# Optimization experiments

Measured on AMD Instinct MI355X. Metric: run time of the kernel, lower is better.

Reference implementation:

```python
import jax, jax.numpy as jnp
import numpy as np

EPS_NORM = 1e-12   # torch F.normalize eps
EPS_BN = 1e-5      # BatchNorm1d eps
NEG_SLOPE = 0.01   # LeakyReLU default


def _l2_normalize(x, axis):
    # torch F.normalize: x / max(||x||, eps)
    n = jnp.sqrt(jnp.sum(x * x, axis=axis, keepdims=True))
    return x / jnp.maximum(n, EPS_NORM)


def setup_inputs() -> dict:
    key = jax.random.key(0)
    k1, k2, k3, k4, k5, k6, k7 = jax.random.split(key, 7)
    B, C, N, M, OUT = 8, 128, 4096, 4096, 128
    return {
        "input": jax.random.normal(k1, (B, C, N), dtype=jnp.float32),
        "target_g": jax.random.normal(k2, (B, C, M), dtype=jnp.float32),
        "weight": jax.random.normal(k3, (C, OUT), dtype=jnp.float32) * (1.0 / np.sqrt(OUT)),
        "gamma": jax.random.normal(k4, (OUT,), dtype=jnp.float32),
        "beta": jax.random.normal(k5, (OUT,), dtype=jnp.float32),
        "running_mean": jax.random.normal(k6, (OUT,), dtype=jnp.float32),
        "running_var": jax.random.uniform(k7, (OUT,), dtype=jnp.float32, minval=0.5, maxval=1.5),
    }


def reference(input, target_g, weight, gamma, beta, running_mean, running_var):
    # input: [B, C, N], target_g: [B, C, M]
    # cosine-similarity adjacency: [B, M, N]
    tg = _l2_normalize(target_g, axis=1)
    inp_n = _l2_normalize(input, axis=1)
    adj = jnp.einsum('bcm,bcn->bmn', tg, inp_n)
    adj = jax.nn.softmax(adj, axis=-1)
    # aggregate: [B, M, C]
    agg = jnp.einsum('bmn,bcn->bmc', adj, input)
    # project: [B, M, OUT] -> permute to [B, OUT, M]
    out = jnp.einsum('bmc,co->bom', agg, weight)
    # LeakyReLU then BatchNorm1d (eval mode, running stats)
    out = jnp.where(out >= 0, out, NEG_SLOPE * out)
    inv = jax.lax.rsqrt(running_var + EPS_BN)
    out = (out - running_mean[None, :, None]) * (inv * gamma)[None, :, None] + beta[None, :, None]
    return out
```

## Files before the change

### kernel.cpp

```cpp
#include <hip/hip_runtime.h>
#include <hip/hip_bf16.h>

#define BATCH 8
#define CDIM 128
#define NDIM 4096

typedef __bf16 bf16x8 __attribute__((ext_vector_type(8)));
typedef float f32x4 __attribute__((ext_vector_type(4)));
typedef float f32x16 __attribute__((ext_vector_type(16)));
typedef unsigned u32x4 __attribute__((ext_vector_type(4)));

#define QT_OFF 0u
#define KT_OFF 8388608u
#define VB_OFF 16777216u
#define WT_OFF 25165824u
#define SC_OFF (WT_OFF + 32768u)
#define BI_OFF (SC_OFF + 512u)

__device__ __forceinline__ f32x4 mfma16(bf16x8 a, bf16x8 b, f32x4 c) {
    return __builtin_amdgcn_mfma_f32_16x16x32_bf16(a, b, c, 0, 0, 0);
}
__device__ __forceinline__ f32x16 mfma32(bf16x8 a, bf16x8 b, f32x16 c) {
    return __builtin_amdgcn_mfma_f32_32x32x16_bf16(a, b, c, 0, 0, 0);
}

__device__ __forceinline__ unsigned pack2bf(float a, float b) {
    unsigned short ul = __builtin_bit_cast(unsigned short, (__bf16)a);
    unsigned short uh = __builtin_bit_cast(unsigned short, (__bf16)b);
    return (unsigned)ul | ((unsigned)uh << 16);
}

__device__ __forceinline__ void glds16(const void* g, void* l) {
    __builtin_amdgcn_global_load_lds((__attribute__((address_space(1))) void*)(void*)g,
                                     (__attribute__((address_space(3))) void*)l, 16, 0, 0);
}

__device__ __forceinline__ void pls32(unsigned& a, unsigned& b) {
    asm("v_permlane32_swap_b32 %0, %1" : "+v"(a), "+v"(b));
}

__global__ __launch_bounds__(256) void prep_nt(const float* __restrict__ input,
                                               const float* __restrict__ tg,
                                               const float* __restrict__ wgt,
                                               const float* __restrict__ gamma,
                                               const float* __restrict__ beta,
                                               const float* __restrict__ mean,
                                               const float* __restrict__ var,
                                               void* __restrict__ ws) {
    __shared__ float Tt[64][129];
    __shared__ float psum[4][64];
    __shared__ float rn[64];
    const int n0 = blockIdx.x * 64;
    const int b  = blockIdx.y;
    const int tid = threadIdx.x;
    const float* src = (blockIdx.z == 0 ? input : tg) + (size_t)b * CDIM * NDIM;

    #pragma unroll
    for (int i = 0; i < 8; ++i) {
        int f = tid + i * 256;
        int c = f >> 4, j4 = f & 15;
        float4 v = *(const float4*)(src + (size_t)c * NDIM + n0 + j4 * 4);
        Tt[j4 * 4 + 0][c] = v.x;
        Tt[j4 * 4 + 1][c] = v.y;
        Tt[j4 * 4 + 2][c] = v.z;
        Tt[j4 * 4 + 3][c] = v.w;
    }
    __syncthreads();
    {
        int j = tid & 63, part = tid >> 6;
        float ss = 0.f;
        #pragma unroll 8
        for (int c = part * 32; c < part * 32 + 32; ++c) { float x = Tt[j][c]; ss += x * x; }
        psum[part][j] = ss;
    }
    __syncthreads();
    if (tid < 64) {
        float s = psum[0][tid] + psum[1][tid] + psum[2][tid] + psum[3][tid];
        rn[tid] = 1.0f / fmaxf(sqrtf(s), 1e-12f);
    }
    __syncthreads();

    __hip_bfloat16* dstT = (__hip_bfloat16*)((char*)ws + (blockIdx.z == 0 ? KT_OFF : QT_OFF))
                           + ((size_t)b * NDIM + n0) * CDIM;
    #pragma unroll
    for (int i = 0; i < 8; ++i) {
        int f = tid + i * 256;
        int j = f >> 5, c4 = f & 31;
        float r = rn[j];
        float4 v = *(const float4*)&Tt[j][c4 * 4];
        uint2 pk; pk.x = pack2bf(v.x * r, v.y * r); pk.y = pack2bf(v.z * r, v.w * r);
        *(uint2*)((unsigned short*)dstT + (size_t)j * CDIM + c4 * 4) = pk;
    }
    if (blockIdx.z == 0) {
        __hip_bfloat16* vb = (__hip_bfloat16*)((char*)ws + VB_OFF) + (size_t)b * CDIM * NDIM + n0;
        #pragma unroll
        for (int i = 0; i < 8; ++i) {
            int f = tid + i * 256;
            int c = f >> 4, j4 = f & 15;
            float x0 = Tt[j4 * 4 + 0][c], x1 = Tt[j4 * 4 + 1][c];
            float x2 = Tt[j4 * 4 + 2][c], x3 = Tt[j4 * 4 + 3][c];
            uint2 pv; pv.x = pack2bf(x0, x1); pv.y = pack2bf(x2, x3);
            *(uint2*)((unsigned short*)vb + (size_t)c * NDIM + j4 * 4) = pv;
        }
    } else if (blockIdx.x == 0 && b == 0) {
        __hip_bfloat16* wT = (__hip_bfloat16*)((char*)ws + WT_OFF);
        float* sc = (float*)((char*)ws + SC_OFF);
        float* bi = (float*)((char*)ws + BI_OFF);
        #pragma unroll
        for (int i = 0; i < 64; ++i) {
            int f = tid + i * 256;
            int c = f >> 7, o = f & 127;
            wT[o * 128 + c] = __hip_bfloat16(wgt[c * 128 + o]);
        }
        if (tid < 128) {
            float inv = rsqrtf(var[tid] + 1e-5f);
            float s = inv * gamma[tid];
            sc[tid] = s;
            bi[tid] = beta[tid] - mean[tid] * s;
        }
    }
}

__global__ __launch_bounds__(512, 2) void flash6(const void* __restrict__ ws_,
                                                 float* __restrict__ out) {
    extern __shared__ char smem[];
    const char* ws = (const char*)ws_;
    const __hip_bfloat16* Qt = (const __hip_bfloat16*)(ws + QT_OFF);
    const __hip_bfloat16* Kt = (const __hip_bfloat16*)(ws + KT_OFF);
    const __hip_bfloat16* Vb = (const __hip_bfloat16*)(ws + VB_OFF);
    const __hip_bfloat16* wT = (const __hip_bfloat16*)(ws + WT_OFF);
    const float* scale = (const float*)(ws + SC_OFF);
    const float* bias  = (const float*)(ws + BI_OFF);

    const int bx = blockIdx.x;
    const int b  = bx & 7;
    const int m0 = (bx >> 3) * 128;
    const int tid = threadIdx.x;
    const int w = tid >> 6, lane = tid & 63;
    const int hf = lane >> 5;
    const int l31 = lane & 31;
    const int nt = w & 1;
    const int mt = w >> 1;

    const char* kgb = (const char*)(Kt + (size_t)b * NDIM * CDIM);
    const char* vgb = (const char*)(Vb + (size_t)b * CDIM * NDIM);

    bf16x8 qb[8];
    {
        const char* qrow = (const char*)Qt + ((size_t)b * NDIM + m0 + mt * 32 + l31) * 256 + hf * 16;
        #pragma unroll
        for (int s = 0; s < 8; ++s) qb[s] = *(const bf16x8*)(qrow + s * 32);
    }

    unsigned kOff[8];
    {
        int nn = nt * 64 + l31;
        #pragma unroll
        for (int s = 0; s < 8; ++s)
            kOff[s] = nn * 256 + (((2 * s + hf) ^ (nn & 15)) * 16);
    }
    unsigned vOff[2][4];
    #pragma unroll
    for (int t = 0; t < 2; ++t)
        #pragma unroll
        for (int ca = 0; ca < 4; ++ca) {
            int c = ca * 32 + l31;
            vOff[t][ca] = 32768 + c * 256 + (((nt * 8 + t * 2 + hf) ^ (c & 15)) * 16);
        }

    const char* kSrc[4]; const char* vSrc[4];
    unsigned kDst[4], vDst[4];
    #pragma unroll
    for (int i = 0; i < 4; ++i) {
        int slot = i * 512 + tid;
        int r = slot >> 4, j = slot & 15;
        kSrc[i] = kgb + r * 256 + ((j ^ (r & 15)) * 16);
        kDst[i] = i * 8192 + w * 1024;
        vSrc[i] = vgb + (size_t)r * 8192 + ((j ^ (r & 15)) * 16);
        vDst[i] = 32768 + i * 8192 + w * 1024;
    }

    f32x16 oacc[4];
    #pragma unroll
    for (int ca = 0; ca < 4; ++ca)
        #pragma unroll
        for (int i = 0; i < 16; ++i) oacc[ca][i] = 0.f;
    float lacc = 0.f;

    #pragma unroll
    for (int i = 0; i < 4; ++i) { glds16(kSrc[i], smem + kDst[i]); kSrc[i] += 32768; }
    #pragma unroll
    for (int i = 0; i < 4; ++i) { glds16(vSrc[i], smem + vDst[i]); vSrc[i] += 256; }

    auto softmax_pf = [&](const f32x16& s, bf16x8* pf) {
        unsigned d[8];
        float lsum = 0.f;
        #pragma unroll
        for (int rq = 0; rq < 4; ++rq) {
            float e0 = __expf(s[rq * 4 + 0] - 1.0f);
            float e1 = __expf(s[rq * 4 + 1] - 1.0f);
            float e2 = __expf(s[rq * 4 + 2] - 1.0f);
            float e3 = __expf(s[rq * 4 + 3] - 1.0f);
            lsum += (e0 + e1) + (e2 + e3);
            d[rq * 2 + 0] = pack2bf(e0, e1);
            d[rq * 2 + 1] = pack2bf(e2, e3);
        }
        lacc += lsum;
        #pragma unroll
        for (int t = 0; t < 2; ++t) {
            pls32(d[4 * t + 0], d[4 * t + 2]);
            pls32(d[4 * t + 1], d[4 * t + 3]);
            u32x4 tv;
            tv.x = d[4 * t + 0]; tv.y = d[4 * t + 1];
            tv.z = d[4 * t + 2]; tv.w = d[4 * t + 3];
            pf[t] = __builtin_bit_cast(bf16x8, tv);
        }
    };

    auto body = [&](const unsigned bo, const bool do_pref) {
        asm volatile("s_waitcnt vmcnt(0) lgkmcnt(0)\ns_barrier" ::: "memory");
        if (do_pref) {
            const unsigned obo = bo ^ 65536u;
            #pragma unroll
            for (int i = 0; i < 4; ++i) { glds16(kSrc[i], smem + (obo + kDst[i])); kSrc[i] += 32768; }
            #pragma unroll
            for (int i = 0; i < 4; ++i) { glds16(vSrc[i], smem + (obo + vDst[i])); vSrc[i] += 256; }
        }
        const char* base = smem + bo;

        f32x16 st0;
        #pragma unroll
        for (int i = 0; i < 16; ++i) st0[i] = 0.f;
        #pragma unroll
        for (int s = 0; s < 8; ++s) {
            bf16x8 kf = *(const bf16x8*)(base + kOff[s]);
            st0 = mfma32(kf, qb[s], st0);
        }
        bf16x8 pf0[2];
        softmax_pf(st0, pf0);

        f32x16 st1;
        #pragma unroll
        for (int i = 0; i < 16; ++i) st1[i] = 0.f;
        #pragma unroll
        for (int s = 0; s < 8; ++s) {
            bf16x8 kf = *(const bf16x8*)(base + kOff[s] + 8192);
            st1 = mfma32(kf, qb[s], st1);
        }

        #pragma unroll
        for (int t = 0; t < 2; ++t)
            #pragma unroll
            for (int ca = 0; ca < 4; ++ca) {
                bf16x8 vf = *(const bf16x8*)(base + vOff[t][ca]);
                oacc[ca] = mfma32(vf, pf0[t], oacc[ca]);
            }

        bf16x8 pf1[2];
        softmax_pf(st1, pf1);

        #pragma unroll
        for (int t = 0; t < 2; ++t)
            #pragma unroll
            for (int ca = 0; ca < 4; ++ca) {
                bf16x8 vf = *(const bf16x8*)(base + (vOff[t][ca] ^ 64u));
                oacc[ca] = mfma32(vf, pf1[t], oacc[ca]);
            }
    };

    for (int ii = 0; ii < 16; ++ii) {
        body(0u, true);
        body(65536u, ii != 15);
    }

    float lw = lacc + __shfl_xor(lacc, 32, 64);
    __syncthreads();
    float* lLds = (float*)(smem + 65536);
    if (lane < 32) lLds[w * 32 + lane] = lw;
    if (w & 1) {
        float4* dst = (float4*)smem + (w >> 1) * 1024 + lane;
        #pragma unroll
        for (int ca = 0; ca < 4; ++ca)
            #pragma unroll
            for (int rq = 0; rq < 4; ++rq) {
                float4 t = { oacc[ca][rq * 4 + 0], oacc[ca][rq * 4 + 1],
                             oacc[ca][rq * 4 + 2], oacc[ca][rq * 4 + 3] };
                dst[(ca * 4 + rq) * 64] = t;
            }
    }
    __syncthreads();
    char* sAgg = smem + 67584;
    if (!(w & 1)) {
        float linv = 1.0f / (lLds[w * 32 + l31] + lLds[(w + 1) * 32 + l31]);
        const float4* srcp = (const float4*)smem + (w >> 1) * 1024 + lane;
        int m = (w >> 1) * 32 + l31;
        char* aggRow = sAgg + m * 256;
        const int mx = (m & 7) << 1;
        #pragma unroll
        for (int ca = 0; ca < 4; ++ca)
            #pragma unroll
            for (int rq = 0; rq < 4; ++rq) {
                float4 ov = srcp[(ca * 4 + rq) * 64];
                float v0 = (oacc[ca][rq * 4 + 0] + ov.x) * linv;
                float v1 = (oacc[ca][rq * 4 + 1] + ov.y) * linv;
                float v2 = (oacc[ca][rq * 4 + 2] + ov.z) * linv;
                float v3 = (oacc[ca][rq * 4 + 3] + ov.w) * linv;
                int cq = ca * 8 + rq * 2 + hf;
                uint2 pk; pk.x = pack2bf(v0, v1); pk.y = pack2bf(v2, v3);
                *(uint2*)(aggRow + ((cq ^ mx) * 8)) = pk;
            }
    }
    __syncthreads();

    const int li = lane & 15, q = lane >> 4;
    const int pm = w * 16 + li;
    f32x4 racc[8];
    #pragma unroll
    for (int ob = 0; ob < 8; ++ob) { racc[ob][0]=0.f; racc[ob][1]=0.f; racc[ob][2]=0.f; racc[ob][3]=0.f; }
    #pragma unroll
    for (int ks = 0; ks < 4; ++ks) {
        int slot8 = ((ks * 4 + q) * 2) ^ ((li & 7) << 1);
        bf16x8 af = *(const bf16x8*)(sAgg + pm * 256 + slot8 * 8);
        #pragma unroll
        for (int ob = 0; ob < 8; ++ob) {
            bf16x8 wf = *(const bf16x8*)((const char*)wT + (ob * 16 + li) * 256 + ks * 64 + q * 16);
            racc[ob] = mfma16(af, wf, racc[ob]);
        }
    }

    float* sRes = (float*)smem;
    #pragma unroll
    for (int ob = 0; ob < 8; ++ob) {
        int oo = ob * 16 + li;
        float sc = scale[oo], bi = bias[oo];
        #pragma unroll
        for (int r = 0; r < 4; ++r) {
            float v = racc[ob][r];
            v = (v >= 0.0f) ? v : 0.01f * v;
            v = v * sc + bi;
            sRes[oo * 132 + w * 16 + q * 4 + r] = v;
        }
    }
    __syncthreads();

    float* outb = out + (size_t)b * CDIM * NDIM + m0;
    #pragma unroll
    for (int i = 0; i < 8; ++i) {
        int f = tid + i * 512;
        int o = f >> 5, mq = f & 31;
        *(float4*)(outb + (size_t)o * NDIM + mq * 4) = *(const float4*)(sRes + o * 132 + mq * 4);
    }
}

extern "C" void kernel_launch(void* const* d_in, const int* in_sizes, int n_in,
                              void* d_out, int out_size, void* d_ws, size_t ws_size,
                              hipStream_t stream) {
    const float* input  = (const float*)d_in[0];
    const float* tg     = (const float*)d_in[1];
    const float* weight = (const float*)d_in[2];
    const float* gamma  = (const float*)d_in[3];
    const float* beta   = (const float*)d_in[4];
    const float* rmean  = (const float*)d_in[5];
    const float* rvar   = (const float*)d_in[6];
    float* out = (float*)d_out;

    (void)in_sizes; (void)n_in; (void)out_size; (void)ws_size;

    hipFuncSetAttribute(reinterpret_cast<const void*>(flash6),
                        hipFuncAttributeMaxDynamicSharedMemorySize, 131072);

    dim3 gprep(NDIM / 64, BATCH, 2);
    prep_nt<<<gprep, 256, 0, stream>>>(input, tg, weight, gamma, beta, rmean, rvar, d_ws);
    flash6<<<dim3(256), 512, 131072, stream>>>(d_ws, out);
}
```

Measured before the change: 181.0 us.

## Double flash kernel block to 1024 threads with 4-way key split per row tile

Doubles the attention kernel's block size to 16 waves, so each 32-row query tile is split across four key sub-ranges instead of two. Each wave now computes one score tile per step instead of two. K/V tiles are stored in LDS in a new unswizzled layout, with each thread issuing half as many global-to-LDS copies. The extra split adds a two-stage cross-wave reduction through LDS and more barriers. The unswizzled LDS layout may cause bank conflicts, and 1024 threads at 128KB LDS can limit occupancy.

```diff
diff --git a/kernel.cpp b/kernel.cpp
--- a/kernel.cpp
+++ b/kernel.cpp
@@ -121,8 +121,8 @@
     }
 }
 
-__global__ __launch_bounds__(512, 2) void flash6(const void* __restrict__ ws_,
-                                                 float* __restrict__ out) {
+__global__ __launch_bounds__(1024, 4) void flash8(const void* __restrict__ ws_,
+                                                  float* __restrict__ out) {
     extern __shared__ char smem[];
     const char* ws = (const char*)ws_;
     const __hip_bfloat16* Qt = (const __hip_bfloat16*)(ws + QT_OFF);
@@ -139,8 +139,8 @@
     const int w = tid >> 6, lane = tid & 63;
     const int hf = lane >> 5;
     const int l31 = lane & 31;
-    const int nt = w & 1;
-    const int mt = w >> 1;
+    const int nt = w & 3;
+    const int mt = w >> 2;
 
     const char* kgb = (const char*)(Kt + (size_t)b * NDIM * CDIM);
     const char* vgb = (const char*)(Vb + (size_t)b * CDIM * NDIM);
@@ -152,33 +152,18 @@
         for (int s = 0; s < 8; ++s) qb[s] = *(const bf16x8*)(qrow + s * 32);
     }
 
-    unsigned kOff[8];
-    {
-        int nn = nt * 64 + l31;
-        #pragma unroll
-        for (int s = 0; s < 8; ++s)
-            kOff[s] = nn * 256 + (((2 * s + hf) ^ (nn & 15)) * 16);
-    }
-    unsigned vOff[2][4];
-    #pragma unroll
-    for (int t = 0; t < 2; ++t)
-        #pragma unroll
-        for (int ca = 0; ca < 4; ++ca) {
-            int c = ca * 32 + l31;
-            vOff[t][ca] = 32768 + c * 256 + (((nt * 8 + t * 2 + hf) ^ (c & 15)) * 16);
-        }
-
-    const char* kSrc[4]; const char* vSrc[4];
-    unsigned kDst[4], vDst[4];
-    #pragma unroll
-    for (int i = 0; i < 4; ++i) {
-        int slot = i * 512 + tid;
-        int r = slot >> 4, j = slot & 15;
-        kSrc[i] = kgb + r * 256 + ((j ^ (r & 15)) * 16);
-        kDst[i] = i * 8192 + w * 1024;
-        vSrc[i] = vgb + (size_t)r * 8192 + ((j ^ (r & 15)) * 16);
-        vDst[i] = 32768 + i * 8192 + w * 1024;
-    }
+    const unsigned kAddr = (nt * 32 + l31) * 16 + hf * 2048;
+    const unsigned vAddr = 65536 + nt * 8192 + hf * 2048 + l31 * 16;
+
+    unsigned kSrcLane[2], vSrcLane[2];
+    #pragma unroll
+    for (int i = 0; i < 2; ++i) {
+        int slot = i * 1024 + tid;
+        int rr = slot & 127, ch = slot >> 7;
+        kSrcLane[i] = rr * 256 + ch * 16;
+        vSrcLane[i] = rr * 8192 + ch * 16;
+    }
+    const unsigned dstU = w * 1024;
 
     f32x16 oacc[4];
     #pragma unroll
@@ -188,9 +173,11 @@
     float lacc = 0.f;
 
     #pragma unroll
-    for (int i = 0; i < 4; ++i) { glds16(kSrc[i], smem + kDst[i]); kSrc[i] += 32768; }
-    #pragma unroll
-    for (int i = 0; i < 4; ++i) { glds16(vSrc[i], smem + vDst[i]); vSrc[i] += 256; }
+    for (int i = 0; i < 2; ++i) glds16(kgb + kSrcLane[i], smem + (i * 16384 + dstU));
+    #pragma unroll
+    for (int i = 0; i < 2; ++i) glds16(vgb + vSrcLane[i], smem + (65536 + i * 16384 + dstU));
+    unsigned kOffG = 32768;
+    unsigned vOffG = 256;
 
     auto softmax_pf = [&](const f32x16& s, bf16x8* pf) {
         unsigned d[8];
@@ -220,65 +207,45 @@
     auto body = [&](const unsigned bo, const bool do_pref) {
         asm volatile("s_waitcnt vmcnt(0) lgkmcnt(0)\ns_barrier" ::: "memory");
         if (do_pref) {
-            const unsigned obo = bo ^ 65536u;
-            #pragma unroll
-            for (int i = 0; i < 4; ++i) { glds16(kSrc[i], smem + (obo + kDst[i])); kSrc[i] += 32768; }
-            #pragma unroll
-            for (int i = 0; i < 4; ++i) { glds16(vSrc[i], smem + (obo + vDst[i])); vSrc[i] += 256; }
-        }
-        const char* base = smem + bo;
-
-        f32x16 st0;
-        #pragma unroll
-        for (int i = 0; i < 16; ++i) st0[i] = 0.f;
+            const unsigned obo = bo ^ 32768u;
+            #pragma unroll
+            for (int i = 0; i < 2; ++i) glds16(kgb + kOffG + kSrcLane[i], smem + (obo + i * 16384 + dstU));
+            #pragma unroll
+            for (int i = 0; i < 2; ++i) glds16(vgb + vOffG + vSrcLane[i], smem + (65536 + obo + i * 16384 + dstU));
+            kOffG += 32768;
+            vOffG += 256;
+        }
+
+        f32x16 st;
+        #pragma unroll
+        for (int i = 0; i < 16; ++i) st[i] = 0.f;
         #pragma unroll
         for (int s = 0; s < 8; ++s) {
-            bf16x8 kf = *(const bf16x8*)(base + kOff[s]);
-            st0 = mfma32(kf, qb[s], st0);
-        }
-        bf16x8 pf0[2];
-        softmax_pf(st0, pf0);
-
-        f32x16 st1;
-        #pragma unroll
-        for (int i = 0; i < 16; ++i) st1[i] = 0.f;
-        #pragma unroll
-        for (int s = 0; s < 8; ++s) {
-            bf16x8 kf = *(const bf16x8*)(base + kOff[s] + 8192);
-            st1 = mfma32(kf, qb[s], st1);
-        }
+            bf16x8 kf = *(const bf16x8*)(smem + bo + kAddr + s * 4096);
+            st = mfma32(kf, qb[s], st);
+        }
+
+        bf16x8 pf[2];
+        softmax_pf(st, pf);
 
         #pragma unroll
         for (int t = 0; t < 2; ++t)
             #pragma unroll
             for (int ca = 0; ca < 4; ++ca) {
-                bf16x8 vf = *(const bf16x8*)(base + vOff[t][ca]);
-                oacc[ca] = mfma32(vf, pf0[t], oacc[ca]);
-            }
-
-        bf16x8 pf1[2];
-        softmax_pf(st1, pf1);
-
-        #pragma unroll
-        for (int t = 0; t < 2; ++t)
-            #pragma unroll
-            for (int ca = 0; ca < 4; ++ca) {
-                bf16x8 vf = *(const bf16x8*)(base + (vOff[t][ca] ^ 64u));
-                oacc[ca] = mfma32(vf, pf1[t], oacc[ca]);
+                bf16x8 vf = *(const bf16x8*)(smem + bo + vAddr + t * 4096 + ca * 512);
+                oacc[ca] = mfma32(vf, pf[t], oacc[ca]);
             }
     };
 
     for (int ii = 0; ii < 16; ++ii) {
         body(0u, true);
-        body(65536u, ii != 15);
+        body(32768u, ii != 15);
     }
 
     float lw = lacc + __shfl_xor(lacc, 32, 64);
     __syncthreads();
-    float* lLds = (float*)(smem + 65536);
-    if (lane < 32) lLds[w * 32 + lane] = lw;
-    if (w & 1) {
-        float4* dst = (float4*)smem + (w >> 1) * 1024 + lane;
+    if (nt >= 2) {
+        float4* dst = (float4*)smem + (mt * 2 + (nt - 2)) * 1024 + lane;
         #pragma unroll
         for (int ca = 0; ca < 4; ++ca)
             #pragma unroll
@@ -289,11 +256,40 @@
             }
     }
     __syncthreads();
+    if (nt < 2) {
+        const float4* srcp = (const float4*)smem + (mt * 2 + nt) * 1024 + lane;
+        #pragma unroll
+        for (int ca = 0; ca < 4; ++ca)
+            #pragma unroll
+            for (int rq = 0; rq < 4; ++rq) {
+                float4 ov = srcp[(ca * 4 + rq) * 64];
+                oacc[ca][rq * 4 + 0] += ov.x;
+                oacc[ca][rq * 4 + 1] += ov.y;
+                oacc[ca][rq * 4 + 2] += ov.z;
+                oacc[ca][rq * 4 + 3] += ov.w;
+            }
+    }
+    __syncthreads();
+    float* lLds = (float*)(smem + 65536);
+    if (lane < 32) lLds[w * 32 + lane] = lw;
+    if (nt == 1) {
+        float4* dst = (float4*)smem + mt * 1024 + lane;
+        #pragma unroll
+        for (int ca = 0; ca < 4; ++ca)
+            #pragma unroll
+            for (int rq = 0; rq < 4; ++rq) {
+                float4 t = { oacc[ca][rq * 4 + 0], oacc[ca][rq * 4 + 1],
+                             oacc[ca][rq * 4 + 2], oacc[ca][rq * 4 + 3] };
+                dst[(ca * 4 + rq) * 64] = t;
+            }
+    }
+    __syncthreads();
     char* sAgg = smem + 67584;
-    if (!(w & 1)) {
-        float linv = 1.0f / (lLds[w * 32 + l31] + lLds[(w + 1) * 32 + l31]);
-        const float4* srcp = (const float4*)smem + (w >> 1) * 1024 + lane;
-        int m = (w >> 1) * 32 + l31;
+    if (nt == 0) {
+        float linv = 1.0f / (lLds[(mt * 4 + 0) * 32 + l31] + lLds[(mt * 4 + 1) * 32 + l31]
+                           + lLds[(mt * 4 + 2) * 32 + l31] + lLds[(mt * 4 + 3) * 32 + l31]);
+        const float4* srcp = (const float4*)smem + mt * 1024 + lane;
+        int m = mt * 32 + l31;
         char* aggRow = sAgg + m * 256;
         const int mx = (m & 7) << 1;
         #pragma unroll
@@ -313,40 +309,42 @@
     __syncthreads();
 
     const int li = lane & 15, q = lane >> 4;
-    const int pm = w * 16 + li;
-    f32x4 racc[8];
-    #pragma unroll
-    for (int ob = 0; ob < 8; ++ob) { racc[ob][0]=0.f; racc[ob][1]=0.f; racc[ob][2]=0.f; racc[ob][3]=0.f; }
-    #pragma unroll
-    for (int ks = 0; ks < 4; ++ks) {
-        int slot8 = ((ks * 4 + q) * 2) ^ ((li & 7) << 1);
-        bf16x8 af = *(const bf16x8*)(sAgg + pm * 256 + slot8 * 8);
+    if (w < 8) {
+        const int pm = w * 16 + li;
+        f32x4 racc[8];
+        #pragma unroll
+        for (int ob = 0; ob < 8; ++ob) { racc[ob][0]=0.f; racc[ob][1]=0.f; racc[ob][2]=0.f; racc[ob][3]=0.f; }
+        #pragma unroll
+        for (int ks = 0; ks < 4; ++ks) {
+            int slot8 = ((ks * 4 + q) * 2) ^ ((li & 7) << 1);
+            bf16x8 af = *(const bf16x8*)(sAgg + pm * 256 + slot8 * 8);
+            #pragma unroll
+            for (int ob = 0; ob < 8; ++ob) {
+                bf16x8 wf = *(const bf16x8*)((const char*)wT + (ob * 16 + li) * 256 + ks * 64 + q * 16);
+                racc[ob] = mfma16(af, wf, racc[ob]);
+            }
+        }
+        float* sRes = (float*)smem;
         #pragma unroll
         for (int ob = 0; ob < 8; ++ob) {
-            bf16x8 wf = *(const bf16x8*)((const char*)wT + (ob * 16 + li) * 256 + ks * 64 + q * 16);
-            racc[ob] = mfma16(af, wf, racc[ob]);
-        }
-    }
-
-    float* sRes = (float*)smem;
-    #pragma unroll
-    for (int ob = 0; ob < 8; ++ob) {
-        int oo = ob * 16 + li;
-        float sc = scale[oo], bi = bias[oo];
-        #pragma unroll
-        for (int r = 0; r < 4; ++r) {
-            float v = racc[ob][r];
-            v = (v >= 0.0f) ? v : 0.01f * v;
-            v = v * sc + bi;
-            sRes[oo * 132 + w * 16 + q * 4 + r] = v;
-        }
-    }
-    __syncthreads();
-
+            int oo = ob * 16 + li;
+            float sc = scale[oo], bi = bias[oo];
+            #pragma unroll
+            for (int r = 0; r < 4; ++r) {
+                float v = racc[ob][r];
+                v = (v >= 0.0f) ? v : 0.01f * v;
+                v = v * sc + bi;
+                sRes[oo * 132 + w * 16 + q * 4 + r] = v;
+            }
+        }
+    }
+    __syncthreads();
+
+    const float* sRes = (const float*)smem;
     float* outb = out + (size_t)b * CDIM * NDIM + m0;
     #pragma unroll
-    for (int i = 0; i < 8; ++i) {
-        int f = tid + i * 512;
+    for (int i = 0; i < 4; ++i) {
+        int f = tid + i * 1024;
         int o = f >> 5, mq = f & 31;
         *(float4*)(outb + (size_t)o * NDIM + mq * 4) = *(const float4*)(sRes + o * 132 + mq * 4);
     }
@@ -366,10 +364,10 @@
 
     (void)in_sizes; (void)n_in; (void)out_size; (void)ws_size;
 
-    hipFuncSetAttribute(reinterpret_cast<const void*>(flash6),
+    hipFuncSetAttribute(reinterpret_cast<const void*>(flash8),
                         hipFuncAttributeMaxDynamicSharedMemorySize, 131072);
 
     dim3 gprep(NDIM / 64, BATCH, 2);
     prep_nt<<<gprep, 256, 0, stream>>>(input, tg, weight, gamma, beta, rmean, rvar, d_ws);
-    flash6<<<dim3(256), 512, 131072, stream>>>(d_ws, out);
-}
+    flash8<<<dim3(256), 1024, 131072, stream>>>(d_ws, out);
+}
```

New measurement: 241.9 us. 33.6% more time.

## Split prep into norm and pack kernels, add MFMA setprio hints

Applied to the files above, without the earlier changes.

The single prep kernel is split in two. A column-norm kernel reads the inputs with coalesced strided loads and writes reciprocal norms into the output buffer, used as scratch. A pack kernel then transposes and writes the bf16 V copy inside its first load loop, which removes the LDS reduction phase and two barriers. The flash kernel raises wave priority around its MFMA loops with s_setprio, so matrix work is favoured over softmax on other waves. The cost is an extra kernel launch and a second full read of the fp32 inputs.

```diff
diff --git a/kernel.cpp b/kernel.cpp
--- a/kernel.cpp
+++ b/kernel.cpp
@@ -39,22 +39,64 @@
     asm("v_permlane32_swap_b32 %0, %1" : "+v"(a), "+v"(b));
 }
 
-__global__ __launch_bounds__(256) void prep_nt(const float* __restrict__ input,
-                                               const float* __restrict__ tg,
-                                               const float* __restrict__ wgt,
-                                               const float* __restrict__ gamma,
-                                               const float* __restrict__ beta,
-                                               const float* __restrict__ mean,
-                                               const float* __restrict__ var,
-                                               void* __restrict__ ws) {
+__global__ __launch_bounds__(256) void prep_norm(const float* __restrict__ input,
+                                                 const float* __restrict__ tg,
+                                                 const float* __restrict__ wgt,
+                                                 const float* __restrict__ gamma,
+                                                 const float* __restrict__ beta,
+                                                 const float* __restrict__ mean,
+                                                 const float* __restrict__ var,
+                                                 float* __restrict__ rn,
+                                                 void* __restrict__ ws) {
+    __shared__ float ps[128];
+    const int b = blockIdx.y, z = blockIdx.z;
+    const int tid = threadIdx.x;
+    const int nl = tid & 127, ch = tid >> 7;
+    const int n = blockIdx.x * 128 + nl;
+    const float* srcp = (z ? tg : input) + ((size_t)b * CDIM + ch * 64) * NDIM + n;
+    float ss = 0.f;
+    #pragma unroll 16
+    for (int c = 0; c < 64; ++c) { float x = srcp[(size_t)c * NDIM]; ss = fmaf(x, x, ss); }
+    if (ch) ps[nl] = ss;
+    __syncthreads();
+    if (!ch) {
+        float t = ss + ps[nl];
+        rn[((size_t)z * BATCH + b) * NDIM + n] = 1.0f / fmaxf(sqrtf(t), 1e-12f);
+    }
+    if (z == 1 && blockIdx.x == 0 && b == 0) {
+        __hip_bfloat16* wT = (__hip_bfloat16*)((char*)ws + WT_OFF);
+        float* sc = (float*)((char*)ws + SC_OFF);
+        float* bi = (float*)((char*)ws + BI_OFF);
+        #pragma unroll 4
+        for (int i = 0; i < 64; ++i) {
+            int f = tid + i * 256;
+            int o = f >> 7, c = f & 127;
+            wT[o * 128 + c] = __hip_bfloat16(wgt[c * 128 + o]);
+        }
+        if (tid < 128) {
+            float inv = rsqrtf(var[tid] + 1e-5f);
+            float s = inv * gamma[tid];
+            sc[tid] = s;
+            bi[tid] = beta[tid] - mean[tid] * s;
+        }
+    }
+}
+
+__global__ __launch_bounds__(256) void prep_pack(const float* __restrict__ input,
+                                                 const float* __restrict__ tg,
+                                                 const float* __restrict__ rn,
+                                                 void* __restrict__ ws) {
     __shared__ float Tt[64][129];
-    __shared__ float psum[4][64];
-    __shared__ float rn[64];
+    __shared__ float rf[64];
     const int n0 = blockIdx.x * 64;
     const int b  = blockIdx.y;
+    const int z  = blockIdx.z;
     const int tid = threadIdx.x;
-    const float* src = (blockIdx.z == 0 ? input : tg) + (size_t)b * CDIM * NDIM;
-
+    const float* src = (z == 0 ? input : tg) + (size_t)b * CDIM * NDIM;
+
+    if (tid < 64) rf[tid] = rn[((size_t)z * BATCH + b) * NDIM + n0 + tid];
+
+    __hip_bfloat16* vb = (__hip_bfloat16*)((char*)ws + VB_OFF) + (size_t)b * CDIM * NDIM + n0;
     #pragma unroll
     for (int i = 0; i < 8; ++i) {
         int f = tid + i * 256;
@@ -64,60 +106,23 @@
         Tt[j4 * 4 + 1][c] = v.y;
         Tt[j4 * 4 + 2][c] = v.z;
         Tt[j4 * 4 + 3][c] = v.w;
-    }
-    __syncthreads();
-    {
-        int j = tid & 63, part = tid >> 6;
-        float ss = 0.f;
-        #pragma unroll 8
-        for (int c = part * 32; c < part * 32 + 32; ++c) { float x = Tt[j][c]; ss += x * x; }
-        psum[part][j] = ss;
-    }
-    __syncthreads();
-    if (tid < 64) {
-        float s = psum[0][tid] + psum[1][tid] + psum[2][tid] + psum[3][tid];
-        rn[tid] = 1.0f / fmaxf(sqrtf(s), 1e-12f);
-    }
-    __syncthreads();
-
-    __hip_bfloat16* dstT = (__hip_bfloat16*)((char*)ws + (blockIdx.z == 0 ? KT_OFF : QT_OFF))
+        if (z == 0) {
+            uint2 pv; pv.x = pack2bf(v.x, v.y); pv.y = pack2bf(v.z, v.w);
+            *(uint2*)((unsigned short*)vb + (size_t)c * NDIM + j4 * 4) = pv;
+        }
+    }
+    __syncthreads();
+
+    __hip_bfloat16* dstT = (__hip_bfloat16*)((char*)ws + (z == 0 ? KT_OFF : QT_OFF))
                            + ((size_t)b * NDIM + n0) * CDIM;
     #pragma unroll
     for (int i = 0; i < 8; ++i) {
         int f = tid + i * 256;
         int j = f >> 5, c4 = f & 31;
-        float r = rn[j];
+        float r = rf[j];
         float4 v = *(const float4*)&Tt[j][c4 * 4];
         uint2 pk; pk.x = pack2bf(v.x * r, v.y * r); pk.y = pack2bf(v.z * r, v.w * r);
         *(uint2*)((unsigned short*)dstT + (size_t)j * CDIM + c4 * 4) = pk;
-    }
-    if (blockIdx.z == 0) {
-        __hip_bfloat16* vb = (__hip_bfloat16*)((char*)ws + VB_OFF) + (size_t)b * CDIM * NDIM + n0;
-        #pragma unroll
-        for (int i = 0; i < 8; ++i) {
-            int f = tid + i * 256;
-            int c = f >> 4, j4 = f & 15;
-            float x0 = Tt[j4 * 4 + 0][c], x1 = Tt[j4 * 4 + 1][c];
-            float x2 = Tt[j4 * 4 + 2][c], x3 = Tt[j4 * 4 + 3][c];
-            uint2 pv; pv.x = pack2bf(x0, x1); pv.y = pack2bf(x2, x3);
-            *(uint2*)((unsigned short*)vb + (size_t)c * NDIM + j4 * 4) = pv;
-        }
-    } else if (blockIdx.x == 0 && b == 0) {
-        __hip_bfloat16* wT = (__hip_bfloat16*)((char*)ws + WT_OFF);
-        float* sc = (float*)((char*)ws + SC_OFF);
-        float* bi = (float*)((char*)ws + BI_OFF);
-        #pragma unroll
-        for (int i = 0; i < 64; ++i) {
-            int f = tid + i * 256;
-            int c = f >> 7, o = f & 127;
-            wT[o * 128 + c] = __hip_bfloat16(wgt[c * 128 + o]);
-        }
-        if (tid < 128) {
-            float inv = rsqrtf(var[tid] + 1e-5f);
-            float s = inv * gamma[tid];
-            sc[tid] = s;
-            bi[tid] = beta[tid] - mean[tid] * s;
-        }
     }
 }
 
@@ -231,17 +236,20 @@
         f32x16 st0;
         #pragma unroll
         for (int i = 0; i < 16; ++i) st0[i] = 0.f;
+        __builtin_amdgcn_s_setprio(1);
         #pragma unroll
         for (int s = 0; s < 8; ++s) {
             bf16x8 kf = *(const bf16x8*)(base + kOff[s]);
             st0 = mfma32(kf, qb[s], st0);
         }
+        __builtin_amdgcn_s_setprio(0);
         bf16x8 pf0[2];
         softmax_pf(st0, pf0);
 
         f32x16 st1;
         #pragma unroll
         for (int i = 0; i < 16; ++i) st1[i] = 0.f;
+        __builtin_amdgcn_s_setprio(1);
         #pragma unroll
         for (int s = 0; s < 8; ++s) {
             bf16x8 kf = *(const bf16x8*)(base + kOff[s] + 8192);
@@ -255,10 +263,12 @@
                 bf16x8 vf = *(const bf16x8*)(base + vOff[t][ca]);
                 oacc[ca] = mfma32(vf, pf0[t], oacc[ca]);
             }
+        __builtin_amdgcn_s_setprio(0);
 
         bf16x8 pf1[2];
         softmax_pf(st1, pf1);
 
+        __builtin_amdgcn_s_setprio(1);
         #pragma unroll
         for (int t = 0; t < 2; ++t)
             #pragma unroll
@@ -266,6 +276,7 @@
                 bf16x8 vf = *(const bf16x8*)(base + (vOff[t][ca] ^ 64u));
                 oacc[ca] = mfma32(vf, pf1[t], oacc[ca]);
             }
+        __builtin_amdgcn_s_setprio(0);
     };
 
     for (int ii = 0; ii < 16; ++ii) {
@@ -369,7 +380,10 @@
     hipFuncSetAttribute(reinterpret_cast<const void*>(flash6),
                         hipFuncAttributeMaxDynamicSharedMemorySize, 131072);
 
-    dim3 gprep(NDIM / 64, BATCH, 2);
-    prep_nt<<<gprep, 256, 0, stream>>>(input, tg, weight, gamma, beta, rmean, rvar, d_ws);
+    float* rnbuf = out;
+
+    prep_norm<<<dim3(NDIM / 128, BATCH, 2), 256, 0, stream>>>(
+        input, tg, weight, gamma, beta, rmean, rvar, rnbuf, d_ws);
+    prep_pack<<<dim3(NDIM / 64, BATCH, 2), 256, 0, stream>>>(input, tg, rnbuf, d_ws);
     flash6<<<dim3(256), 512, 131072, stream>>>(d_ws, out);
 }
```

New measurement: 187.1 us. 3.4% more time.

## Fuse prep and flash kernels into one cooperative launch with grid sync

Applied to the files above, without the earlier changes.

Merges the normalization/transpose prep kernel into the main attention kernel. Each of the 256 blocks now processes four 64-column prep tiles, then all blocks meet at a cooperative grid-wide barrier before the flash stage. This removes a kernel launch and the gap between the two kernels. In exchange, the prep work runs on only 256 blocks instead of 1024 and needs a grid barrier, which may lower memory parallelism in the prep phase.

```diff
diff --git a/kernel.cpp b/kernel.cpp
--- a/kernel.cpp
+++ b/kernel.cpp
@@ -1,5 +1,8 @@
 #include <hip/hip_runtime.h>
 #include <hip/hip_bf16.h>
+#include <hip/hip_cooperative_groups.h>
+
+namespace cg = cooperative_groups;
 
 #define BATCH 8
 #define CDIM 128
@@ -39,92 +42,110 @@
     asm("v_permlane32_swap_b32 %0, %1" : "+v"(a), "+v"(b));
 }
 
-__global__ __launch_bounds__(256) void prep_nt(const float* __restrict__ input,
-                                               const float* __restrict__ tg,
-                                               const float* __restrict__ wgt,
-                                               const float* __restrict__ gamma,
-                                               const float* __restrict__ beta,
-                                               const float* __restrict__ mean,
-                                               const float* __restrict__ var,
-                                               void* __restrict__ ws) {
-    __shared__ float Tt[64][129];
-    __shared__ float psum[4][64];
-    __shared__ float rn[64];
-    const int n0 = blockIdx.x * 64;
-    const int b  = blockIdx.y;
+__global__ __launch_bounds__(512, 2) void fused(const float* __restrict__ input,
+                                                const float* __restrict__ tg,
+                                                const float* __restrict__ wgt,
+                                                const float* __restrict__ gamma,
+                                                const float* __restrict__ beta,
+                                                const float* __restrict__ mean,
+                                                const float* __restrict__ var,
+                                                void* __restrict__ wsv,
+                                                float* __restrict__ out) {
+    extern __shared__ char smem[];
+    char* ws = (char*)wsv;
+    const int bx = blockIdx.x;
+    const int b  = bx & 7;
     const int tid = threadIdx.x;
-    const float* src = (blockIdx.z == 0 ? input : tg) + (size_t)b * CDIM * NDIM;
-
-    #pragma unroll
-    for (int i = 0; i < 8; ++i) {
-        int f = tid + i * 256;
-        int c = f >> 4, j4 = f & 15;
-        float4 v = *(const float4*)(src + (size_t)c * NDIM + n0 + j4 * 4);
-        Tt[j4 * 4 + 0][c] = v.x;
-        Tt[j4 * 4 + 1][c] = v.y;
-        Tt[j4 * 4 + 2][c] = v.z;
-        Tt[j4 * 4 + 3][c] = v.w;
-    }
-    __syncthreads();
+
     {
-        int j = tid & 63, part = tid >> 6;
-        float ss = 0.f;
-        #pragma unroll 8
-        for (int c = part * 32; c < part * 32 + 32; ++c) { float x = Tt[j][c]; ss += x * x; }
-        psum[part][j] = ss;
-    }
-    __syncthreads();
-    if (tid < 64) {
-        float s = psum[0][tid] + psum[1][tid] + psum[2][tid] + psum[3][tid];
-        rn[tid] = 1.0f / fmaxf(sqrtf(s), 1e-12f);
-    }
-    __syncthreads();
-
-    __hip_bfloat16* dstT = (__hip_bfloat16*)((char*)ws + (blockIdx.z == 0 ? KT_OFF : QT_OFF))
-                           + ((size_t)b * NDIM + n0) * CDIM;
-    #pragma unroll
-    for (int i = 0; i < 8; ++i) {
-        int f = tid + i * 256;
-        int j = f >> 5, c4 = f & 31;
-        float r = rn[j];
-        float4 v = *(const float4*)&Tt[j][c4 * 4];
-        uint2 pk; pk.x = pack2bf(v.x * r, v.y * r); pk.y = pack2bf(v.z * r, v.w * r);
-        *(uint2*)((unsigned short*)dstT + (size_t)j * CDIM + c4 * 4) = pk;
-    }
-    if (blockIdx.z == 0) {
-        __hip_bfloat16* vb = (__hip_bfloat16*)((char*)ws + VB_OFF) + (size_t)b * CDIM * NDIM + n0;
-        #pragma unroll
-        for (int i = 0; i < 8; ++i) {
-            int f = tid + i * 256;
-            int c = f >> 4, j4 = f & 15;
-            float x0 = Tt[j4 * 4 + 0][c], x1 = Tt[j4 * 4 + 1][c];
-            float x2 = Tt[j4 * 4 + 2][c], x3 = Tt[j4 * 4 + 3][c];
-            uint2 pv; pv.x = pack2bf(x0, x1); pv.y = pack2bf(x2, x3);
-            *(uint2*)((unsigned short*)vb + (size_t)c * NDIM + j4 * 4) = pv;
-        }
-    } else if (blockIdx.x == 0 && b == 0) {
-        __hip_bfloat16* wT = (__hip_bfloat16*)((char*)ws + WT_OFF);
-        float* sc = (float*)((char*)ws + SC_OFF);
-        float* bi = (float*)((char*)ws + BI_OFF);
-        #pragma unroll
-        for (int i = 0; i < 64; ++i) {
-            int f = tid + i * 256;
-            int c = f >> 7, o = f & 127;
-            wT[o * 128 + c] = __hip_bfloat16(wgt[c * 128 + o]);
-        }
-        if (tid < 128) {
-            float inv = rsqrtf(var[tid] + 1e-5f);
-            float s = inv * gamma[tid];
-            sc[tid] = s;
-            bi[tid] = beta[tid] - mean[tid] * s;
-        }
-    }
-}
-
-__global__ __launch_bounds__(512, 2) void flash6(const void* __restrict__ ws_,
-                                                 float* __restrict__ out) {
-    extern __shared__ char smem[];
-    const char* ws = (const char*)ws_;
+        float* Tt   = (float*)smem;
+        float* psum = (float*)(smem + 33024);
+        float* rnl  = (float*)(smem + 35072);
+        const int g = bx >> 3;
+
+        for (int k = 0; k < 4; ++k) {
+            const int m  = g * 4 + k;
+            const int z  = m >> 6;
+            const int n0 = (m & 63) * 64;
+            const float* src = (z ? tg : input) + (size_t)b * CDIM * NDIM;
+
+            #pragma unroll
+            for (int i = 0; i < 4; ++i) {
+                int f = tid + i * 512;
+                int c = f >> 4, j4 = f & 15;
+                float4 v = *(const float4*)(src + (size_t)c * NDIM + n0 + j4 * 4);
+                Tt[(j4 * 4 + 0) * 129 + c] = v.x;
+                Tt[(j4 * 4 + 1) * 129 + c] = v.y;
+                Tt[(j4 * 4 + 2) * 129 + c] = v.z;
+                Tt[(j4 * 4 + 3) * 129 + c] = v.w;
+            }
+            __syncthreads();
+            {
+                int j = tid & 63, part = tid >> 6;
+                float ss = 0.f;
+                #pragma unroll 8
+                for (int c = part * 16; c < part * 16 + 16; ++c) {
+                    float x = Tt[j * 129 + c];
+                    ss = fmaf(x, x, ss);
+                }
+                psum[part * 64 + j] = ss;
+            }
+            __syncthreads();
+            if (tid < 64) {
+                float s = 0.f;
+                #pragma unroll
+                for (int p = 0; p < 8; ++p) s += psum[p * 64 + tid];
+                rnl[tid] = 1.0f / fmaxf(sqrtf(s), 1e-12f);
+            }
+            __syncthreads();
+
+            __hip_bfloat16* dstT = (__hip_bfloat16*)(ws + (z == 0 ? KT_OFF : QT_OFF))
+                                   + ((size_t)b * NDIM + n0) * CDIM;
+            #pragma unroll
+            for (int i = 0; i < 4; ++i) {
+                int f = tid + i * 512;
+                int j = f >> 5, c4 = f & 31;
+                float r = rnl[j];
+                float4 v = *(const float4*)&Tt[j * 129 + c4 * 4];
+                uint2 pk; pk.x = pack2bf(v.x * r, v.y * r); pk.y = pack2bf(v.z * r, v.w * r);
+                *(uint2*)((unsigned short*)dstT + (size_t)j * CDIM + c4 * 4) = pk;
+            }
+            if (z == 0) {
+                __hip_bfloat16* vb = (__hip_bfloat16*)(ws + VB_OFF) + (size_t)b * CDIM * NDIM + n0;
+                #pragma unroll
+                for (int i = 0; i < 4; ++i) {
+                    int f = tid + i * 512;
+                    int c = f >> 4, j4 = f & 15;
+                    float x0 = Tt[(j4 * 4 + 0) * 129 + c], x1 = Tt[(j4 * 4 + 1) * 129 + c];
+                    float x2 = Tt[(j4 * 4 + 2) * 129 + c], x3 = Tt[(j4 * 4 + 3) * 129 + c];
+                    uint2 pv; pv.x = pack2bf(x0, x1); pv.y = pack2bf(x2, x3);
+                    *(uint2*)((unsigned short*)vb + (size_t)c * NDIM + j4 * 4) = pv;
+                }
+            }
+            __syncthreads();
+        }
+
+        if (bx == 0) {
+            __hip_bfloat16* wT = (__hip_bfloat16*)(ws + WT_OFF);
+            float* sc = (float*)(ws + SC_OFF);
+            float* bi = (float*)(ws + BI_OFF);
+            #pragma unroll 4
+            for (int i = 0; i < 32; ++i) {
+                int f = tid + i * 512;
+                int c = f >> 7, o = f & 127;
+                wT[o * 128 + c] = __hip_bfloat16(wgt[c * 128 + o]);
+            }
+            if (tid < 128) {
+                float inv = rsqrtf(var[tid] + 1e-5f);
+                float s = inv * gamma[tid];
+                sc[tid] = s;
+                bi[tid] = beta[tid] - mean[tid] * s;
+            }
+        }
+    }
+
+    cg::this_grid().sync();
+
     const __hip_bfloat16* Qt = (const __hip_bfloat16*)(ws + QT_OFF);
     const __hip_bfloat16* Kt = (const __hip_bfloat16*)(ws + KT_OFF);
     const __hip_bfloat16* Vb = (const __hip_bfloat16*)(ws + VB_OFF);
@@ -132,10 +153,7 @@
     const float* scale = (const float*)(ws + SC_OFF);
     const float* bias  = (const float*)(ws + BI_OFF);
 
-    const int bx = blockIdx.x;
-    const int b  = bx & 7;
     const int m0 = (bx >> 3) * 128;
-    const int tid = threadIdx.x;
     const int w = tid >> 6, lane = tid & 63;
     const int hf = lane >> 5;
     const int l31 = lane & 31;
@@ -366,10 +384,12 @@
 
     (void)in_sizes; (void)n_in; (void)out_size; (void)ws_size;
 
-    hipFuncSetAttribute(reinterpret_cast<const void*>(flash6),
+    hipFuncSetAttribute(reinterpret_cast<const void*>(fused),
                         hipFuncAttributeMaxDynamicSharedMemorySize, 131072);
 
-    dim3 gprep(NDIM / 64, BATCH, 2);
-    prep_nt<<<gprep, 256, 0, stream>>>(input, tg, weight, gamma, beta, rmean, rvar, d_ws);
-    flash6<<<dim3(256), 512, 131072, stream>>>(d_ws, out);
-}
+    void* args[] = { (void*)&input, (void*)&tg, (void*)&weight, (void*)&gamma,
+                     (void*)&beta, (void*)&rmean, (void*)&rvar, (void*)&d_ws,
+                     (void*)&out };
+    hipLaunchCooperativeKernel(reinterpret_cast<const void*>(fused),
+                               dim3(256), dim3(512), args, 131072, stream);
+}
```

New measurement: 237.6 us. +31.2%, slower.
